# Performance work log

Hardware: AMD Instinct MI355X
Metric: run time of the kernel (lower is better)

## Reference

```python
import jax, jax.numpy as jnp
import numpy as np

N = 100000   # nodes
E = 1600000  # edges (avg degree 16)
D = 256      # in_channels == dim (forward hard-codes BatchNorm1d(256))
BN_EPS = 1e-5


def _batchnorm(x, gamma, beta):
    # training-mode BatchNorm1d: batch statistics over node dim, biased variance
    mu = jnp.mean(x, axis=0)
    var = jnp.var(x, axis=0)
    return (x - mu) * jax.lax.rsqrt(var + BN_EPS) * gamma + beta


def _gin_conv(x, src, dst, n, W1, b1, gamma, beta, W2, b2):
    # GINConv, eps=0: nn((1+eps)*x + sum_{j in N(i)} x_j)
    agg = jax.ops.segment_sum(x[src], dst, num_segments=n)  # sparse neighbor sum
    h = x + agg
    h = jax.nn.relu(_batchnorm(h @ W1 + b1, gamma, beta))
    return jax.nn.relu(h @ W2 + b2)


def setup_inputs() -> dict:
    key = jax.random.key(0)
    ks = jax.random.split(key, 8)
    x = jax.random.normal(ks[0], (N, D), dtype=jnp.float32)
    edge_index = jax.random.randint(ks[1], (2, E), 0, N, dtype=jnp.int64)
    s = 0.02
    inp = {
        "x": x,
        "edge_index": edge_index,
        # fresh BatchNorm1d(256) in forward (default affine params)
        "g0": jnp.ones((D,), jnp.float32),
        "b0": jnp.zeros((D,), jnp.float32),
        # conv1 MLP: Linear-BN-ReLU-Linear-ReLU
        "W1a": jax.random.normal(ks[2], (D, D), jnp.float32) * s,
        "b1a": jnp.zeros((D,), jnp.float32),
        "g1": jnp.ones((D,), jnp.float32),
        "bt1": jnp.zeros((D,), jnp.float32),
        "W1b": jax.random.normal(ks[3], (D, D), jnp.float32) * s,
        "b1b": jnp.zeros((D,), jnp.float32),
        # conv2 MLP
        "W2a": jax.random.normal(ks[4], (D, D), jnp.float32) * s,
        "b2a": jnp.zeros((D,), jnp.float32),
        "g2": jnp.ones((D,), jnp.float32),
        "bt2": jnp.zeros((D,), jnp.float32),
        "W2b": jax.random.normal(ks[5], (D, D), jnp.float32) * s,
        "b2b": jnp.zeros((D,), jnp.float32),
    }
    return inp


def reference(x, edge_index, g0, b0, W1a, b1a, g1, bt1, W1b, b1b,
              W2a, b2a, g2, bt2, W2b, b2b):
    n = x.shape[0]
    src, dst = edge_index[0], edge_index[1]
    h = _batchnorm(x, g0, b0)                       # fresh BN(256) on input
    h = _gin_conv(h, src, dst, n, W1a, b1a, g1, bt1, W1b, b1b)
    h = jax.nn.relu(h)                              # outer relu (dropout=eval, identity)
    h = _gin_conv(h, src, dst, n, W2a, b2a, g2, bt2, W2b, b2b)
    return jax.nn.relu(h)
```

## Files before the change

### kernel.cpp

```cpp
#include <hip/hip_runtime.h>

#define N_NODES 100000
#define N_EDGES 1600000
#define DIM 256
#define NBINS 196
#define BINCAP 16384

typedef unsigned short bf16u;
typedef __attribute__((ext_vector_type(8))) short bf16x8s;
typedef __attribute__((ext_vector_type(4))) float f32x4;

__device__ __forceinline__ float bf2f(unsigned int u16) {
    union { unsigned int i; float f; } x; x.i = u16 << 16; return x.f;
}
__device__ __forceinline__ float hi2f(unsigned int u) {
    union { unsigned int i; float f; } x; x.i = u & 0xffff0000u; return x.f;
}
__device__ __forceinline__ float lo2f(unsigned int u) {
    union { unsigned int i; float f; } x; x.i = u << 16; return x.f;
}
__device__ __forceinline__ bf16u f2bf(float f) {
    union { float f; unsigned int i; } x; x.f = f;
    unsigned int i = x.i;
    return (bf16u)((i + 0x7fffu + ((i >> 16) & 1u)) >> 16);
}
__device__ __forceinline__ float loadv(const void* p, size_t i, int isf32) {
    return isf32 ? ((const float*)p)[i] : bf2f(((const bf16u*)p)[i]);
}
__device__ __forceinline__ void async_copy16(const void* g, void* l) {
    __builtin_amdgcn_global_load_lds((const __attribute__((address_space(1))) void*)g,
                                     (__attribute__((address_space(3))) void*)l, 16, 0, 0);
}

__global__ void detect_flags(const unsigned* xw, const int* ei, int* flags, int* gBinFill,
                             float* sums) {
    __shared__ int cnt, nz;
    if (threadIdx.x == 0) { cnt = 0; nz = 0; }
    __syncthreads();
    gBinFill[threadIdx.x] = 0;
#pragma unroll
    for (int i = 0; i < 6; ++i) sums[i * 256 + threadIdx.x] = 0.f;
    unsigned u = xw[threadIdx.x];
    float av = fabsf(bf2f(u & 0xffffu));
    if (av > 1e-5f && av < 50.f) atomicAdd(&cnt, 1);
    if (ei[2 * threadIdx.x + 1] != 0) atomicAdd(&nz, 1);
    __syncthreads();
    if (threadIdx.x == 0) {
        flags[0] = (cnt >= 128) ? 0 : 1;
        if (nz == 0) { flags[1] = 2; flags[2] = 2 * N_EDGES; }
        else         { flags[1] = 1; flags[2] = N_EDGES; }
    }
}

__global__ void transpose_w(const void* W0, const void* W1, const void* W2, const void* W3,
                            bf16u* Wt, const int* flags) {
    __shared__ bf16u tile[64][65];
    int isf32 = flags[0];
    const void* W = (blockIdx.y == 0) ? W0 : (blockIdx.y == 1) ? W1 : (blockIdx.y == 2) ? W2 : W3;
    bf16u* out = Wt + (size_t)blockIdx.y * DIM * DIM;
    int t = threadIdx.x;
    int tx = t & 63, ty = t >> 6;
    int k0 = (blockIdx.x >> 2) * 64, n0 = (blockIdx.x & 3) * 64;
#pragma unroll
    for (int i = 0; i < 16; ++i) {
        int r = ty + i * 4;
        tile[tx][r] = f2bf(loadv(W, (size_t)(k0 + r) * DIM + (n0 + tx), isf32));
    }
    __syncthreads();
#pragma unroll
    for (int i = 0; i < 16; ++i) {
        int r = ty + i * 4;
        out[(size_t)(n0 + r) * DIM + (k0 + tx)] = tile[r][tx];
    }
}

__global__ __launch_bounds__(256) void bin_scatter(const int* __restrict__ ei,
                                                   const int* __restrict__ flags,
                                                   uint2* __restrict__ gRec,
                                                   int* __restrict__ gBinFill) {
    __shared__ int cnt[256];
    __shared__ int cur[256];
    __shared__ uint2 rec[4096];
    int t = threadIdx.x;
    cnt[t] = 0; cur[t] = 0;
    __syncthreads();
    int st = flags[1], ofs = flags[2];
    int e0 = blockIdx.x * 4096;
#pragma unroll
    for (int i = 0; i < 16; ++i) {
        int e = e0 + i * 256 + t;
        uint2 r;
        if (e < N_EDGES) {
            r.x = (unsigned)ei[(size_t)ofs + (size_t)e * st];
            r.y = (unsigned)ei[(size_t)e * st];
            atomicAdd(&cnt[r.x >> 9], 1);
        } else {
            r.x = 0xffffffffu; r.y = 0;
        }
        rec[i * 256 + t] = r;
    }
    __syncthreads();
    if (t < NBINS) {
        int c = cnt[t];
        int b = (c > 0) ? atomicAdd(&gBinFill[t], c) : 0;
        cnt[t] = b;
    }
    __syncthreads();
#pragma unroll
    for (int i = 0; i < 16; ++i) {
        uint2 r = rec[i * 256 + t];
        if (r.x != 0xffffffffu) {
            int b = r.x >> 9;
            int li = atomicAdd(&cur[b], 1);
            int pos = cnt[b] + li;
            if (pos < BINCAP) gRec[(size_t)b * BINCAP + pos] = r;
        }
    }
}

__global__ void bin_scan(const int* gBinFill, int* binBase) {
    __shared__ int s[256];
    int t = threadIdx.x;
    s[t] = (t < NBINS) ? gBinFill[t] : 0;
    __syncthreads();
    for (int off = 1; off < 256; off <<= 1) {
        int v = (t >= off) ? s[t - off] : 0;
        __syncthreads();
        s[t] += v;
        __syncthreads();
    }
    binBase[t + 1] = s[t];
    if (t == 0) binBase[0] = 0;
}

__global__ __launch_bounds__(256) void bin_csr(const uint2* __restrict__ gRec,
                                               const int* __restrict__ gBinFill,
                                               const int* __restrict__ binBase,
                                               int* __restrict__ rp, int* __restrict__ col) {
    __shared__ int cntA[512], scanB[512], noff[512], ncur[512];
    int bin = blockIdx.x, t = threadIdx.x;
    int cnt = gBinFill[bin];
    if (cnt > BINCAP) cnt = BINCAP;
    int gbase = binBase[bin], lo = bin << 9;
    cntA[t] = 0; cntA[t + 256] = 0; ncur[t] = 0; ncur[t + 256] = 0;
    __syncthreads();
    const uint2* R = gRec + (size_t)bin * BINCAP;
    for (int j = t; j < cnt; j += 256) atomicAdd(&cntA[(int)R[j].x - lo], 1);
    __syncthreads();
    scanB[t] = cntA[t]; scanB[t + 256] = cntA[t + 256];
    __syncthreads();
    for (int off = 1; off < 512; off <<= 1) {
        int v0 = (t >= off) ? scanB[t - off] : 0;
        int v1 = (t + 256 >= off) ? scanB[t + 256 - off] : 0;
        __syncthreads();
        scanB[t] += v0; scanB[t + 256] += v1;
        __syncthreads();
    }
    noff[t] = scanB[t] - cntA[t];
    noff[t + 256] = scanB[t + 256] - cntA[t + 256];
    __syncthreads();
    int n0 = lo + t, n1 = lo + t + 256;
    if (n0 < N_NODES) rp[n0] = gbase + noff[t];
    if (n1 < N_NODES) rp[n1] = gbase + noff[t + 256];
    if (bin == 0 && t == 0) rp[N_NODES] = N_EDGES;
    for (int j = t; j < cnt; j += 256) {
        uint2 r = R[j];
        int k = (int)r.x - lo;
        int li = atomicAdd(&ncur[k], 1);
        col[gbase + noff[k] + li] = (int)r.y;
    }
}

__global__ void col_stats(const void* X, int nrows, float* sums, const int* flags, int dual) {
    __shared__ float ls[512];
    int isf32 = dual ? flags[0] : 0;
    int t = threadIdx.x;
    ls[t] = 0.f; ls[t + 256] = 0.f;
    __syncthreads();
    int rpb = (nrows + gridDim.x - 1) / gridDim.x;
    int r0 = blockIdx.x * rpb;
    int r1 = r0 + rpb; if (r1 > nrows) r1 = nrows;
    int cg = (t & 31) * 8;
    float s[8], q[8];
#pragma unroll
    for (int j = 0; j < 8; ++j) { s[j] = 0.f; q[j] = 0.f; }
    if (isf32) {
        for (int r = r0 + (t >> 5); r < r1; r += 8) {
            const float* xp = (const float*)X + (size_t)r * DIM + cg;
            f32x4 a = *(const f32x4*)xp, b = *(const f32x4*)(xp + 4);
#pragma unroll
            for (int j = 0; j < 4; ++j) {
                s[j] += a[j]; q[j] += a[j] * a[j];
                s[4 + j] += b[j]; q[4 + j] += b[j] * b[j];
            }
        }
    } else {
        for (int r = r0 + (t >> 5); r < r1; r += 8) {
            size_t base = (size_t)r * DIM + cg;
#pragma unroll
            for (int j = 0; j < 8; ++j) {
                float f = bf2f(((const bf16u*)X)[base + j]);
                s[j] += f; q[j] += f * f;
            }
        }
    }
#pragma unroll
    for (int j = 0; j < 8; ++j) {
        atomicAdd(&ls[cg + j], s[j]);
        atomicAdd(&ls[256 + cg + j], q[j]);
    }
    __syncthreads();
    atomicAdd(&sums[t], ls[t]);
    atomicAdd(&sums[256 + t], ls[256 + t]);
}

__global__ void bn_finalize(const float* sums, const void* gamma, const void* beta,
                            float* sc, float* sh, float inv_n, const int* flags) {
    int isf32 = flags[0];
    int t = threadIdx.x;
    float mu = sums[t] * inv_n;
    float var = sums[256 + t] * inv_n - mu * mu;
    float rs = rsqrtf(var + 1e-5f);
    float g = loadv(gamma, t, isf32), b = loadv(beta, t, isf32);
    sc[t] = rs * g;
    sh[t] = b - mu * rs * g;
}

__global__ void bn_apply(const void* X, const float* sc, const float* sh, bf16u* Y,
                         const int* flags, int dual, int relu) {
    int isf32 = dual ? flags[0] : 0;
    size_t i = (size_t)blockIdx.x * 256 + threadIdx.x;
    int c = ((int)(i & 31)) * 8;
    size_t base = i * 8;
    float v[8];
    if (isf32) {
        f32x4 x0 = *(const f32x4*)((const float*)X + base);
        f32x4 x1 = *(const f32x4*)((const float*)X + base + 4);
#pragma unroll
        for (int j = 0; j < 4; ++j) { v[j] = x0[j]; v[4 + j] = x1[j]; }
    } else {
        uint4 u = *(const uint4*)((const bf16u*)X + base);
        v[0] = lo2f(u.x); v[1] = hi2f(u.x);
        v[2] = lo2f(u.y); v[3] = hi2f(u.y);
        v[4] = lo2f(u.z); v[5] = hi2f(u.z);
        v[6] = lo2f(u.w); v[7] = hi2f(u.w);
    }
    f32x4 s0 = *(const f32x4*)(sc + c), s1 = *(const f32x4*)(sc + c + 4);
    f32x4 h0 = *(const f32x4*)(sh + c), h1 = *(const f32x4*)(sh + c + 4);
    float y[8];
#pragma unroll
    for (int j = 0; j < 4; ++j) {
        y[j]     = v[j]     * s0[j] + h0[j];
        y[4 + j] = v[4 + j] * s1[j] + h1[j];
    }
    if (relu) {
#pragma unroll
        for (int j = 0; j < 8; ++j) y[j] = fmaxf(y[j], 0.f);
    }
    uint4 ov;
    ov.x = (unsigned)f2bf(y[0]) | ((unsigned)f2bf(y[1]) << 16);
    ov.y = (unsigned)f2bf(y[2]) | ((unsigned)f2bf(y[3]) << 16);
    ov.z = (unsigned)f2bf(y[4]) | ((unsigned)f2bf(y[5]) << 16);
    ov.w = (unsigned)f2bf(y[6]) | ((unsigned)f2bf(y[7]) << 16);
    *(uint4*)(Y + base) = ov;
}

__global__ __launch_bounds__(256) void aggregate(const bf16u* __restrict__ h,
                                                 const int* __restrict__ rp,
                                                 const int* __restrict__ col,
                                                 bf16u* __restrict__ out) {
    int node = blockIdx.x * 4 + (threadIdx.x >> 6);
    int lane = threadIdx.x & 63;
    int p = lane >> 5, c = lane & 31;
    const uint4* hv = (const uint4*)h;
    float acc[8];
    if (p == 0) {
        uint4 u = hv[(size_t)node * 32 + c];
        acc[0] = lo2f(u.x); acc[1] = hi2f(u.x);
        acc[2] = lo2f(u.y); acc[3] = hi2f(u.y);
        acc[4] = lo2f(u.z); acc[5] = hi2f(u.z);
        acc[6] = lo2f(u.w); acc[7] = hi2f(u.w);
    } else {
#pragma unroll
        for (int j = 0; j < 8; ++j) acc[j] = 0.f;
    }
    int e = rp[node], e1 = rp[node + 1];
    for (; e + 8 <= e1; e += 8) {
        int s0 = col[e + p], s1 = col[e + 2 + p], s2 = col[e + 4 + p], s3 = col[e + 6 + p];
        uint4 a = hv[(size_t)s0 * 32 + c];
        uint4 b = hv[(size_t)s1 * 32 + c];
        uint4 d = hv[(size_t)s2 * 32 + c];
        uint4 f = hv[(size_t)s3 * 32 + c];
        acc[0] += lo2f(a.x); acc[1] += hi2f(a.x); acc[2] += lo2f(a.y); acc[3] += hi2f(a.y);
        acc[4] += lo2f(a.z); acc[5] += hi2f(a.z); acc[6] += lo2f(a.w); acc[7] += hi2f(a.w);
        acc[0] += lo2f(b.x); acc[1] += hi2f(b.x); acc[2] += lo2f(b.y); acc[3] += hi2f(b.y);
        acc[4] += lo2f(b.z); acc[5] += hi2f(b.z); acc[6] += lo2f(b.w); acc[7] += hi2f(b.w);
        acc[0] += lo2f(d.x); acc[1] += hi2f(d.x); acc[2] += lo2f(d.y); acc[3] += hi2f(d.y);
        acc[4] += lo2f(d.z); acc[5] += hi2f(d.z); acc[6] += lo2f(d.w); acc[7] += hi2f(d.w);
        acc[0] += lo2f(f.x); acc[1] += hi2f(f.x); acc[2] += lo2f(f.y); acc[3] += hi2f(f.y);
        acc[4] += lo2f(f.z); acc[5] += hi2f(f.z); acc[6] += lo2f(f.w); acc[7] += hi2f(f.w);
    }
    for (; e + 4 <= e1; e += 4) {
        int s0 = col[e + p], s1 = col[e + 2 + p];
        uint4 a = hv[(size_t)s0 * 32 + c];
        uint4 b = hv[(size_t)s1 * 32 + c];
        acc[0] += lo2f(a.x); acc[1] += hi2f(a.x); acc[2] += lo2f(a.y); acc[3] += hi2f(a.y);
        acc[4] += lo2f(a.z); acc[5] += hi2f(a.z); acc[6] += lo2f(a.w); acc[7] += hi2f(a.w);
        acc[0] += lo2f(b.x); acc[1] += hi2f(b.x); acc[2] += lo2f(b.y); acc[3] += hi2f(b.y);
        acc[4] += lo2f(b.z); acc[5] += hi2f(b.z); acc[6] += lo2f(b.w); acc[7] += hi2f(b.w);
    }
    for (; e < e1; e += 2) {
        int idx = e + p;
        if (idx < e1) {
            uint4 a = hv[(size_t)col[idx] * 32 + c];
            acc[0] += lo2f(a.x); acc[1] += hi2f(a.x); acc[2] += lo2f(a.y); acc[3] += hi2f(a.y);
            acc[4] += lo2f(a.z); acc[5] += hi2f(a.z); acc[6] += lo2f(a.w); acc[7] += hi2f(a.w);
        }
    }
#pragma unroll
    for (int j = 0; j < 8; ++j) acc[j] += __shfl_xor(acc[j], 32);
    if (p == 0) {
        uint4 ov;
        ov.x = (unsigned)f2bf(acc[0]) | ((unsigned)f2bf(acc[1]) << 16);
        ov.y = (unsigned)f2bf(acc[2]) | ((unsigned)f2bf(acc[3]) << 16);
        ov.z = (unsigned)f2bf(acc[4]) | ((unsigned)f2bf(acc[5]) << 16);
        ov.w = (unsigned)f2bf(acc[6]) | ((unsigned)f2bf(acc[7]) << 16);
        ((uint4*)out)[(size_t)node * 32 + c] = ov;
    }
}

__global__ __launch_bounds__(256) void gemm_bias(const bf16u* __restrict__ A,
                                                 const bf16u* __restrict__ Wt,
                                                 const void* __restrict__ bias,
                                                 void* __restrict__ Cout, int mrows,
                                                 const int* __restrict__ flags,
                                                 int relu, int f32out,
                                                 float* __restrict__ stats,
                                                 const float* __restrict__ bnsc,
                                                 const float* __restrict__ bnsh) {
    __shared__ bf16u As[128 * 64];
    __shared__ bf16u Bs[128 * 64];
    __shared__ float lsum[256];
    int isf32 = flags[0];
    int t = threadIdx.x;
    int w = t >> 6, lane = t & 63;
    int lr = lane & 15, lq = lane >> 4;
    int wm = w >> 1, wn = w & 1;
    int xcd = blockIdx.x & 7, j0 = blockIdx.x >> 3;
    int wkid = ((xcd < 4) ? xcd * 196 : 784 + (xcd - 4) * 195) + j0;
    int rowBase = (wkid >> 1) * 128, colBase = (wkid & 1) * 128;
    f32x4 acc[4][4] = {};
    lsum[t] = 0.f;
    int srow = t >> 3;
    int g8   = ((t & 7) ^ ((t >> 3) & 7)) * 8;
    for (int k0 = 0; k0 < 256; k0 += 64) {
        __syncthreads();
        if (bnsc) {
            f32x4 s0v = *(const f32x4*)(bnsc + k0 + g8);
            f32x4 s1v = *(const f32x4*)(bnsc + k0 + g8 + 4);
            f32x4 h0v = *(const f32x4*)(bnsh + k0 + g8);
            f32x4 h1v = *(const f32x4*)(bnsh + k0 + g8 + 4);
#pragma unroll
            for (int p = 0; p < 4; ++p) {
                int r = p * 32 + srow;
                int gr = rowBase + r; gr = (gr < mrows) ? gr : (mrows - 1);
                uint4 av = *(const uint4*)(A + (size_t)gr * 256 + k0 + g8);
                float y0 = fmaxf(lo2f(av.x) * s0v[0] + h0v[0], 0.f);
                float y1 = fmaxf(hi2f(av.x) * s0v[1] + h0v[1], 0.f);
                float y2 = fmaxf(lo2f(av.y) * s0v[2] + h0v[2], 0.f);
                float y3 = fmaxf(hi2f(av.y) * s0v[3] + h0v[3], 0.f);
                float y4 = fmaxf(lo2f(av.z) * s1v[0] + h1v[0], 0.f);
                float y5 = fmaxf(hi2f(av.z) * s1v[1] + h1v[1], 0.f);
                float y6 = fmaxf(lo2f(av.w) * s1v[2] + h1v[2], 0.f);
                float y7 = fmaxf(hi2f(av.w) * s1v[3] + h1v[3], 0.f);
                uint4 ov;
                ov.x = (unsigned)f2bf(y0) | ((unsigned)f2bf(y1) << 16);
                ov.y = (unsigned)f2bf(y2) | ((unsigned)f2bf(y3) << 16);
                ov.z = (unsigned)f2bf(y4) | ((unsigned)f2bf(y5) << 16);
                ov.w = (unsigned)f2bf(y6) | ((unsigned)f2bf(y7) << 16);
                *(uint4*)&As[r * 64 + (t & 7) * 8] = ov;
                async_copy16(Wt + (size_t)(colBase + r) * 256 + k0 + g8,
                             &Bs[(p * 32 + (w << 3)) * 64]);
            }
        } else {
#pragma unroll
            for (int p = 0; p < 4; ++p) {
                int r = p * 32 + srow;
                int gr = rowBase + r; gr = (gr < mrows) ? gr : (mrows - 1);
                async_copy16(A + (size_t)gr * 256 + k0 + g8, &As[(p * 32 + (w << 3)) * 64]);
                async_copy16(Wt + (size_t)(colBase + r) * 256 + k0 + g8,
                             &Bs[(p * 32 + (w << 3)) * 64]);
            }
        }
        __syncthreads();
#pragma unroll
        for (int ks = 0; ks < 2; ++ks) {
            bf16x8s af[4], bfv[4];
#pragma unroll
            for (int mt = 0; mt < 4; ++mt) {
                int ar = wm * 64 + mt * 16 + lr;
                af[mt] = *(const bf16x8s*)&As[ar * 64 + (((ks * 4 + lq) ^ (lr & 7)) * 8)];
            }
#pragma unroll
            for (int nt = 0; nt < 4; ++nt) {
                int br = wn * 64 + nt * 16 + lr;
                bfv[nt] = *(const bf16x8s*)&Bs[br * 64 + (((ks * 4 + lq) ^ (lr & 7)) * 8)];
            }
#pragma unroll
            for (int mt = 0; mt < 4; ++mt)
#pragma unroll
                for (int nt = 0; nt < 4; ++nt)
                    acc[mt][nt] = __builtin_amdgcn_mfma_f32_16x16x32_bf16(af[mt], bfv[nt], acc[mt][nt], 0, 0, 0);
        }
    }
    int storef32 = f32out && isf32;
#pragma unroll
    for (int nt = 0; nt < 4; ++nt) {
        int cl = wn * 64 + nt * 16 + lr;
        int c = colBase + cl;
        float bv = loadv(bias, c, isf32);
        float ssum = 0.f, ssq = 0.f;
#pragma unroll
        for (int mt = 0; mt < 4; ++mt) {
            int r0 = rowBase + wm * 64 + mt * 16 + lq * 4;
#pragma unroll
            for (int j = 0; j < 4; ++j) {
                int r = r0 + j;
                if (r < mrows) {
                    float y = acc[mt][nt][j] + bv;
                    if (relu) y = fmaxf(y, 0.f);
                    if (storef32) ((float*)Cout)[(size_t)r * 256 + c] = y;
                    else          ((bf16u*)Cout)[(size_t)r * 256 + c] = f2bf(y);
                    ssum += y; ssq += y * y;
                }
            }
        }
        if (stats) {
            atomicAdd(&lsum[cl], ssum);
            atomicAdd(&lsum[128 + cl], ssq);
        }
    }
    if (stats) {
        __syncthreads();
        if (t < 128) {
            atomicAdd(&stats[colBase + t], lsum[t]);
            atomicAdd(&stats[256 + colBase + t], lsum[128 + t]);
        }
    }
}

extern "C" void kernel_launch(void* const* d_in, const int* in_sizes, int n_in,
                              void* d_out, int out_size, void* d_ws, size_t ws_size,
                              hipStream_t stream) {
    const void* x   = d_in[0];
    const int*  ei  = (const int*)d_in[1];
    const void* g0  = d_in[2];
    const void* b0  = d_in[3];
    const void* W1a = d_in[4];
    const void* b1a = d_in[5];
    const void* g1  = d_in[6];
    const void* bt1 = d_in[7];
    const void* W1b = d_in[8];
    const void* b1b = d_in[9];
    const void* W2a = d_in[10];
    const void* b2a = d_in[11];
    const void* g2  = d_in[12];
    const void* bt2 = d_in[13];
    const void* W2b = d_in[14];
    const void* b2b = d_in[15];

    char* ws = (char*)d_ws;
    size_t off = 0;
    auto alloc = [&](size_t bytes) {
        char* p = ws + off;
        off += (bytes + 255) & ~(size_t)255;
        return p;
    };
    const size_t FB = (size_t)N_NODES * DIM * 2;
    bf16u* bufA  = (bf16u*)alloc(FB);
    bf16u* bufB  = (bf16u*)alloc(FB);
    bf16u* Wt    = (bf16u*)alloc((size_t)4 * DIM * DIM * 2);
    int*   colA  = (int*)alloc((size_t)N_EDGES * 4);
    int*   rp    = (int*)alloc((size_t)(N_NODES + 1) * 4);
    int*   gBinFill = (int*)alloc(256 * 4);
    int*   binBase  = (int*)alloc(260 * 4);
    float* sums0 = (float*)alloc(512 * 4);
    float* sums1 = (float*)alloc(512 * 4);
    float* sums2 = (float*)alloc(512 * 4);
    float* sc    = (float*)alloc(256 * 4);
    float* sh    = (float*)alloc(256 * 4);
    int*   flags = (int*)alloc(4 * 4);

    uint2* gRec = (uint2*)bufB;

    bf16u* Wt1a = Wt;
    bf16u* Wt1b = Wt + 65536;
    bf16u* Wt2a = Wt + 2 * 65536;
    bf16u* Wt2b = Wt + 3 * 65536;

    const float inv_n = 1.0f / (float)N_NODES;

    detect_flags<<<1, 256, 0, stream>>>((const unsigned*)x, ei, flags, gBinFill, sums0);
    transpose_w<<<dim3(16, 4), 256, 0, stream>>>(W1a, W1b, W2a, W2b, Wt, flags);

    bin_scatter<<<391, 256, 0, stream>>>(ei, flags, gRec, gBinFill);
    bin_scan<<<1, 256, 0, stream>>>(gBinFill, binBase);
    bin_csr<<<NBINS, 256, 0, stream>>>(gRec, gBinFill, binBase, rp, colA);

    col_stats<<<500, 256, 0, stream>>>(x, N_NODES, sums0, flags, 1);
    bn_finalize<<<1, 256, 0, stream>>>(sums0, g0, b0, sc, sh, inv_n, flags);
    bn_apply<<<12500, 256, 0, stream>>>(x, sc, sh, bufB, flags, 1, 0);

    aggregate<<<25000, 256, 0, stream>>>(bufB, rp, colA, bufA);
    gemm_bias<<<1564, 256, 0, stream>>>(bufA, Wt1a, b1a, bufB, N_NODES, flags, 0, 0, sums1,
                                        nullptr, nullptr);
    bn_finalize<<<1, 256, 0, stream>>>(sums1, g1, bt1, sc, sh, inv_n, flags);
    gemm_bias<<<1564, 256, 0, stream>>>(bufB, Wt1b, b1b, bufA, N_NODES, flags, 1, 0, nullptr,
                                        sc, sh);

    aggregate<<<25000, 256, 0, stream>>>(bufA, rp, colA, bufB);
    gemm_bias<<<1564, 256, 0, stream>>>(bufB, Wt2a, b2a, bufA, N_NODES, flags, 0, 0, sums2,
                                        nullptr, nullptr);
    bn_finalize<<<1, 256, 0, stream>>>(sums2, g2, bt2, sc, sh, inv_n, flags);
    gemm_bias<<<1564, 256, 0, stream>>>(bufA, Wt2b, b2b, d_out, N_NODES, flags, 1, 1, nullptr,
                                        sc, sh);
}
```

Measured before the change: 824.8 us.

## Double-buffer LDS tiles in gemm_bias to prefetch next K-slice during MFMA

The GEMM now keeps two LDS buffers for the A and B tiles. While the current 64-wide K slice runs through MFMA, it issues the async copies for the next slice, or, on the BN-fused path, loads A into registers and applies the scale/shift/ReLU afterwards. This cuts one barrier per K iteration and overlaps global loads with math. The cost is doubled LDS use, which may reduce occupancy, and extra registers for the prefetched A values.

```diff
diff --git a/kernel.cpp b/kernel.cpp
--- a/kernel.cpp
+++ b/kernel.cpp
@@ -338,8 +338,8 @@
                                                  float* __restrict__ stats,
                                                  const float* __restrict__ bnsc,
                                                  const float* __restrict__ bnsh) {
-    __shared__ bf16u As[128 * 64];
-    __shared__ bf16u Bs[128 * 64];
+    __shared__ bf16u As[2][128 * 64];
+    __shared__ bf16u Bs[2][128 * 64];
     __shared__ float lsum[256];
     int isf32 = flags[0];
     int t = threadIdx.x;
@@ -353,58 +353,83 @@
     lsum[t] = 0.f;
     int srow = t >> 3;
     int g8   = ((t & 7) ^ ((t >> 3) & 7)) * 8;
-    for (int k0 = 0; k0 < 256; k0 += 64) {
+    int ldsOff = (t >> 3) * 64 + (t & 7) * 8;
+
+    if (bnsc) {
+        f32x4 s0v = *(const f32x4*)(bnsc + g8);
+        f32x4 s1v = *(const f32x4*)(bnsc + g8 + 4);
+        f32x4 h0v = *(const f32x4*)(bnsh + g8);
+        f32x4 h1v = *(const f32x4*)(bnsh + g8 + 4);
+#pragma unroll
+        for (int p = 0; p < 4; ++p) {
+            int r = p * 32 + srow;
+            int gr = rowBase + r; gr = (gr < mrows) ? gr : (mrows - 1);
+            uint4 av = *(const uint4*)(A + (size_t)gr * 256 + g8);
+            uint4 ov;
+            ov.x = (unsigned)f2bf(fmaxf(lo2f(av.x) * s0v[0] + h0v[0], 0.f)) |
+                   ((unsigned)f2bf(fmaxf(hi2f(av.x) * s0v[1] + h0v[1], 0.f)) << 16);
+            ov.y = (unsigned)f2bf(fmaxf(lo2f(av.y) * s0v[2] + h0v[2], 0.f)) |
+                   ((unsigned)f2bf(fmaxf(hi2f(av.y) * s0v[3] + h0v[3], 0.f)) << 16);
+            ov.z = (unsigned)f2bf(fmaxf(lo2f(av.z) * s1v[0] + h1v[0], 0.f)) |
+                   ((unsigned)f2bf(fmaxf(hi2f(av.z) * s1v[1] + h1v[1], 0.f)) << 16);
+            ov.w = (unsigned)f2bf(fmaxf(lo2f(av.w) * s1v[2] + h1v[2], 0.f)) |
+                   ((unsigned)f2bf(fmaxf(hi2f(av.w) * s1v[3] + h1v[3], 0.f)) << 16);
+            *(uint4*)&As[0][p * 2048 + ldsOff] = ov;
+            async_copy16(Wt + (size_t)(colBase + r) * 256 + g8, &Bs[0][(p * 32 + (w << 3)) * 64]);
+        }
+    } else {
+#pragma unroll
+        for (int p = 0; p < 4; ++p) {
+            int r = p * 32 + srow;
+            int gr = rowBase + r; gr = (gr < mrows) ? gr : (mrows - 1);
+            async_copy16(A + (size_t)gr * 256 + g8, &As[0][(p * 32 + (w << 3)) * 64]);
+            async_copy16(Wt + (size_t)(colBase + r) * 256 + g8, &Bs[0][(p * 32 + (w << 3)) * 64]);
+        }
+    }
+
+    for (int kt = 0; kt < 4; ++kt) {
+        int b = kt & 1, bn = b ^ 1;
+        int kn = (kt + 1) * 64;
         __syncthreads();
-        if (bnsc) {
-            f32x4 s0v = *(const f32x4*)(bnsc + k0 + g8);
-            f32x4 s1v = *(const f32x4*)(bnsc + k0 + g8 + 4);
-            f32x4 h0v = *(const f32x4*)(bnsh + k0 + g8);
-            f32x4 h1v = *(const f32x4*)(bnsh + k0 + g8 + 4);
-#pragma unroll
-            for (int p = 0; p < 4; ++p) {
-                int r = p * 32 + srow;
-                int gr = rowBase + r; gr = (gr < mrows) ? gr : (mrows - 1);
-                uint4 av = *(const uint4*)(A + (size_t)gr * 256 + k0 + g8);
-                float y0 = fmaxf(lo2f(av.x) * s0v[0] + h0v[0], 0.f);
-                float y1 = fmaxf(hi2f(av.x) * s0v[1] + h0v[1], 0.f);
-                float y2 = fmaxf(lo2f(av.y) * s0v[2] + h0v[2], 0.f);
-                float y3 = fmaxf(hi2f(av.y) * s0v[3] + h0v[3], 0.f);
-                float y4 = fmaxf(lo2f(av.z) * s1v[0] + h1v[0], 0.f);
-                float y5 = fmaxf(hi2f(av.z) * s1v[1] + h1v[1], 0.f);
-                float y6 = fmaxf(lo2f(av.w) * s1v[2] + h1v[2], 0.f);
-                float y7 = fmaxf(hi2f(av.w) * s1v[3] + h1v[3], 0.f);
-                uint4 ov;
-                ov.x = (unsigned)f2bf(y0) | ((unsigned)f2bf(y1) << 16);
-                ov.y = (unsigned)f2bf(y2) | ((unsigned)f2bf(y3) << 16);
-                ov.z = (unsigned)f2bf(y4) | ((unsigned)f2bf(y5) << 16);
-                ov.w = (unsigned)f2bf(y6) | ((unsigned)f2bf(y7) << 16);
-                *(uint4*)&As[r * 64 + (t & 7) * 8] = ov;
-                async_copy16(Wt + (size_t)(colBase + r) * 256 + k0 + g8,
-                             &Bs[(p * 32 + (w << 3)) * 64]);
-            }
-        } else {
-#pragma unroll
-            for (int p = 0; p < 4; ++p) {
-                int r = p * 32 + srow;
-                int gr = rowBase + r; gr = (gr < mrows) ? gr : (mrows - 1);
-                async_copy16(A + (size_t)gr * 256 + k0 + g8, &As[(p * 32 + (w << 3)) * 64]);
-                async_copy16(Wt + (size_t)(colBase + r) * 256 + k0 + g8,
-                             &Bs[(p * 32 + (w << 3)) * 64]);
-            }
-        }
-        __syncthreads();
+        uint4 av[4];
+        if (kt < 3) {
+            if (bnsc) {
+#pragma unroll
+                for (int p = 0; p < 4; ++p) {
+                    int r = p * 32 + srow;
+                    int gr = rowBase + r; gr = (gr < mrows) ? gr : (mrows - 1);
+                    av[p] = *(const uint4*)(A + (size_t)gr * 256 + kn + g8);
+                }
+#pragma unroll
+                for (int p = 0; p < 4; ++p) {
+                    int r = p * 32 + srow;
+                    async_copy16(Wt + (size_t)(colBase + r) * 256 + kn + g8,
+                                 &Bs[bn][(p * 32 + (w << 3)) * 64]);
+                }
+            } else {
+#pragma unroll
+                for (int p = 0; p < 4; ++p) {
+                    int r = p * 32 + srow;
+                    int gr = rowBase + r; gr = (gr < mrows) ? gr : (mrows - 1);
+                    async_copy16(A + (size_t)gr * 256 + kn + g8,
+                                 &As[bn][(p * 32 + (w << 3)) * 64]);
+                    async_copy16(Wt + (size_t)(colBase + r) * 256 + kn + g8,
+                                 &Bs[bn][(p * 32 + (w << 3)) * 64]);
+                }
+            }
+        }
 #pragma unroll
         for (int ks = 0; ks < 2; ++ks) {
             bf16x8s af[4], bfv[4];
 #pragma unroll
             for (int mt = 0; mt < 4; ++mt) {
                 int ar = wm * 64 + mt * 16 + lr;
-                af[mt] = *(const bf16x8s*)&As[ar * 64 + (((ks * 4 + lq) ^ (lr & 7)) * 8)];
+                af[mt] = *(const bf16x8s*)&As[b][ar * 64 + (((ks * 4 + lq) ^ (lr & 7)) * 8)];
             }
 #pragma unroll
             for (int nt = 0; nt < 4; ++nt) {
                 int br = wn * 64 + nt * 16 + lr;
-                bfv[nt] = *(const bf16x8s*)&Bs[br * 64 + (((ks * 4 + lq) ^ (lr & 7)) * 8)];
+                bfv[nt] = *(const bf16x8s*)&Bs[b][br * 64 + (((ks * 4 + lq) ^ (lr & 7)) * 8)];
             }
 #pragma unroll
             for (int mt = 0; mt < 4; ++mt)
@@ -412,7 +437,27 @@
                 for (int nt = 0; nt < 4; ++nt)
                     acc[mt][nt] = __builtin_amdgcn_mfma_f32_16x16x32_bf16(af[mt], bfv[nt], acc[mt][nt], 0, 0, 0);
         }
-    }
+        if (bnsc && kt < 3) {
+            f32x4 s0v = *(const f32x4*)(bnsc + kn + g8);
+            f32x4 s1v = *(const f32x4*)(bnsc + kn + g8 + 4);
+            f32x4 h0v = *(const f32x4*)(bnsh + kn + g8);
+            f32x4 h1v = *(const f32x4*)(bnsh + kn + g8 + 4);
+#pragma unroll
+            for (int p = 0; p < 4; ++p) {
+                uint4 ov;
+                ov.x = (unsigned)f2bf(fmaxf(lo2f(av[p].x) * s0v[0] + h0v[0], 0.f)) |
+                       ((unsigned)f2bf(fmaxf(hi2f(av[p].x) * s0v[1] + h0v[1], 0.f)) << 16);
+                ov.y = (unsigned)f2bf(fmaxf(lo2f(av[p].y) * s0v[2] + h0v[2], 0.f)) |
+                       ((unsigned)f2bf(fmaxf(hi2f(av[p].y) * s0v[3] + h0v[3], 0.f)) << 16);
+                ov.z = (unsigned)f2bf(fmaxf(lo2f(av[p].z) * s1v[0] + h1v[0], 0.f)) |
+                       ((unsigned)f2bf(fmaxf(hi2f(av[p].z) * s1v[1] + h1v[1], 0.f)) << 16);
+                ov.w = (unsigned)f2bf(fmaxf(lo2f(av[p].w) * s1v[2] + h1v[2], 0.f)) |
+                       ((unsigned)f2bf(fmaxf(hi2f(av[p].w) * s1v[3] + h1v[3], 0.f)) << 16);
+                *(uint4*)&As[bn][p * 2048 + ldsOff] = ov;
+            }
+        }
+    }
+
     int storef32 = f32out && isf32;
 #pragma unroll
     for (int nt = 0; nt < 4; ++nt) {
```

Result: no change. 824.8 us (+0.0%).
